# Optimization experiments

Hardware: AMD Instinct MI355X
Metric: run time of the kernel (lower is better)

The kernel has to match this reference:

```python
import jax, jax.numpy as jnp
import numpy as np

B, C, S = 32768, 30, 7
COORD, NOOBJ = 5.0, 0.5


def setup_inputs() -> dict:
    key = jax.random.key(0)
    k1, k2, k3 = jax.random.split(key, 3)
    # uniform in [0.05, 1): size loss takes sqrt of raw channels, so keep them positive
    pre = jax.random.uniform(k1, (B, C, S, S), jnp.float32, 0.05, 1.0)
    lab = jax.random.uniform(k2, (B, C, S, S), jnp.float32, 0.05, 1.0)
    # channel 4 of the label is a binary objectness indicator (code tests == 1)
    objm = (jax.random.uniform(k3, (B, S, S)) < 0.3).astype(jnp.float32)
    lab = lab.at[:, 4].set(objm)
    return {"pre": pre, "lab": lab}


def _iou(b1, b2):
    # b1, b2: [B, 4, S, S] with channels (x1, y1, x2, y2); original '+1' pixel convention
    ix1 = jnp.maximum(b1[:, 0], b2[:, 0])
    iy1 = jnp.maximum(b1[:, 1], b2[:, 1])
    ix2 = jnp.minimum(b1[:, 2], b2[:, 2])
    iy2 = jnp.minimum(b1[:, 3], b2[:, 3])
    inter = jnp.maximum(ix2 - ix1 + 1.0, 0.0) * jnp.maximum(iy2 - iy1 + 1.0, 0.0)
    a1 = (b1[:, 2] - b1[:, 0] + 1.0) * (b1[:, 3] - b1[:, 1] + 1.0)
    a2 = (b2[:, 2] - b2[:, 0] + 1.0) * (b2[:, 3] - b2[:, 1] + 1.0)
    return inter / (a1 + a2 - inter)


def reference(pre, lab):
    obj = lab[:, 4] == 1.0                      # [B,S,S] objectness mask
    iou1 = _iou(pre[:, 0:4], lab[:, 0:4])       # box 1 IoU
    iou2 = _iou(pre[:, 5:9], lab[:, 5:9])       # box 2 IoU
    resp1 = iou1 >= iou2                        # box 1 responsible

    # coordinate loss: the px*64 / py*64 grid offsets cancel in (cxl - cxp)
    addr1 = COORD * ((lab[:, 0] - pre[:, 0]) ** 2 + (lab[:, 1] - pre[:, 1]) ** 2)
    addr2 = COORD * ((lab[:, 5] - pre[:, 5]) ** 2 + (lab[:, 6] - pre[:, 6]) ** 2)

    size1 = COORD * ((jnp.sqrt(pre[:, 2]) - jnp.sqrt(lab[:, 2])) ** 2
                     + (jnp.sqrt(pre[:, 3]) - jnp.sqrt(lab[:, 3])) ** 2)
    size2 = COORD * ((jnp.sqrt(pre[:, 7]) - jnp.sqrt(lab[:, 7])) ** 2
                     + (jnp.sqrt(pre[:, 8]) - jnp.sqrt(lab[:, 8])) ** 2)

    # original always uses pre[9] as the responsible confidence (faithful to source)
    conf = NOOBJ * (pre[:, 9] - jnp.where(resp1, iou1, iou2)) ** 2

    obj_terms = jnp.where(resp1, addr1 + size1, addr2 + size2) + conf
    noobj_terms = NOOBJ * (pre[:, 4] + pre[:, 9]) ** 2

    # class loss is accumulated for every cell regardless of objectness
    cls = jnp.sum((pre[:, 10:] - lab[:, 10:]) ** 2)

    total = jnp.sum(jnp.where(obj, obj_terms, noobj_terms)) + cls
    return total / B
```

## Files before the change

### kernel.cpp

```cpp
#include <hip/hip_runtime.h>


#define BATCH   32768
#define S2      49
#define CPB     1470
#define NB      2
#define GFLOATS (NB * CPB)
#define GVEC    (GFLOATS / 4)
#define NGROUPS (BATCH / NB)
#define CELLS   (NB * S2)
#define NBLK    1536

__device__ __forceinline__ float iou4(float px1, float py1, float px2, float py2,
                                      float lx1, float ly1, float lx2, float ly2) {
    float ix1 = fmaxf(px1, lx1), iy1 = fmaxf(py1, ly1);
    float ix2 = fminf(px2, lx2), iy2 = fminf(py2, ly2);
    float iw = fmaxf(ix2 - ix1 + 1.0f, 0.0f);
    float ih = fmaxf(iy2 - iy1 + 1.0f, 0.0f);
    float inter = iw * ih;
    float a1 = (px2 - px1 + 1.0f) * (py2 - py1 + 1.0f);
    float a2 = (lx2 - lx1 + 1.0f) * (ly2 - ly1 + 1.0f);
    return inter / (a1 + a2 - inter);
}

__global__ __launch_bounds__(256) void yolo_loss_main(const float4* __restrict__ pre4,
                                                      const float4* __restrict__ lab4,
                                                      float* __restrict__ partials) {
    __shared__ float4 smem[2 * GVEC];
    __shared__ float red[4];
    float* preS = (float*)smem;
    float* labS = (float*)(smem + GVEC);
    const int tid = threadIdx.x;

    float acc = 0.0f;
    for (int g = blockIdx.x; g < NGROUPS; g += gridDim.x) {
        const float4* __restrict__ ps = pre4 + (size_t)g * GVEC;
        const float4* __restrict__ ls = lab4 + (size_t)g * GVEC;
        #pragma unroll
        for (int k = 0; k < 3; ++k) {
            int i = tid + k * 256;
            if (i < GVEC) {
                smem[i]        = ps[i];
                smem[GVEC + i] = ls[i];
            }
        }
        __syncthreads();

        if (tid < CELLS) {
            int bl = tid / S2;
            int s  = tid - bl * S2;
            const float* __restrict__ P = preS + bl * CPB + s;
            const float* __restrict__ L = labS + bl * CPB + s;

            float p0 = P[0],      p1 = P[S2],     p2 = P[2 * S2], p3 = P[3 * S2], p4 = P[4 * S2];
            float p5 = P[5 * S2], p6 = P[6 * S2], p7 = P[7 * S2], p8 = P[8 * S2], p9 = P[9 * S2];
            float l0 = L[0],      l1 = L[S2],     l2 = L[2 * S2], l3 = L[3 * S2], l4 = L[4 * S2];
            float l5 = L[5 * S2], l6 = L[6 * S2], l7 = L[7 * S2], l8 = L[8 * S2];

            float iou1 = iou4(p0, p1, p2, p3, l0, l1, l2, l3);
            float iou2 = iou4(p5, p6, p7, p8, l5, l6, l7, l8);
            bool resp1 = iou1 >= iou2;

            float d0 = l0 - p0, d1 = l1 - p1, d5 = l5 - p5, d6 = l6 - p6;
            float addr1 = 5.0f * (d0 * d0 + d1 * d1);
            float addr2 = 5.0f * (d5 * d5 + d6 * d6);

            float e2 = sqrtf(p2) - sqrtf(l2), e3 = sqrtf(p3) - sqrtf(l3);
            float e7 = sqrtf(p7) - sqrtf(l7), e8 = sqrtf(p8) - sqrtf(l8);
            float size1 = 5.0f * (e2 * e2 + e3 * e3);
            float size2 = 5.0f * (e7 * e7 + e8 * e8);

            float du = p9 - (resp1 ? iou1 : iou2);
            float conf = 0.5f * du * du;

            float obj_terms = (resp1 ? (addr1 + size1) : (addr2 + size2)) + conf;
            float pn = p4 + p9;
            float noobj = 0.5f * pn * pn;
            float cellv = (l4 == 1.0f) ? obj_terms : noobj;

            float cls = 0.0f;
            #pragma unroll
            for (int c = 10; c < 30; ++c) {
                float d = P[c * S2] - L[c * S2];
                cls += d * d;
            }
            acc += cellv + cls;
        }
        __syncthreads();
    }

    #pragma unroll
    for (int off = 32; off > 0; off >>= 1) acc += __shfl_down(acc, off);
    int lane = tid & 63, wid = tid >> 6;
    if (lane == 0) red[wid] = acc;
    __syncthreads();
    if (tid == 0) partials[blockIdx.x] = red[0] + red[1] + red[2] + red[3];
}

__global__ __launch_bounds__(256) void yolo_loss_final(const float* __restrict__ partials,
                                                       int n, float* __restrict__ out) {
    double v = 0.0;
    for (int i = (int)threadIdx.x; i < n; i += 256) v += (double)partials[i];
    __shared__ double sm[256];
    sm[threadIdx.x] = v;
    __syncthreads();
    for (int s = 128; s > 0; s >>= 1) {
        if ((int)threadIdx.x < s) sm[threadIdx.x] += sm[threadIdx.x + s];
        __syncthreads();
    }
    if (threadIdx.x == 0) out[0] = (float)(sm[0] * (1.0 / (double)BATCH));
}

extern "C" void kernel_launch(void* const* d_in, const int* in_sizes, int n_in,
                              void* d_out, int out_size, void* d_ws, size_t ws_size,
                              hipStream_t stream) {
    const float4* pre4 = (const float4*)d_in[0];
    const float4* lab4 = (const float4*)d_in[1];
    float* out = (float*)d_out;
    float* partials = (float*)d_ws;

    int nblk = NBLK;
    if (ws_size < (size_t)nblk * sizeof(float)) {
        nblk = (int)(ws_size / sizeof(float));
        if (nblk < 1) nblk = 1;
    }

    yolo_loss_main<<<nblk, 256, 0, stream>>>(pre4, lab4, partials);
    yolo_loss_final<<<1, 256, 0, stream>>>(partials, nblk, out);
}
```

Baseline: 73.01 us.

## Double-buffer LDS, stage only box channels, reduce class terms in registers

```diff
diff --git a/kernel.cpp b/kernel.cpp
--- a/kernel.cpp
+++ b/kernel.cpp
@@ -5,11 +5,13 @@
 #define S2      49
 #define CPB     1470
 #define NB      2
-#define GFLOATS (NB * CPB)
-#define GVEC    (GFLOATS / 4)
+#define GF      (NB * CPB)
+#define GV      (GF / 4)
 #define NGROUPS (BATCH / NB)
-#define CELLS   (NB * S2)
-#define NBLK    1536
+#define LDSB    492
+#define HALF    (NB * LDSB)
+#define BUFSZ   (2 * HALF)
+#define NBLK    2048
 
 __device__ __forceinline__ float iou4(float px1, float py1, float px2, float py2,
                                       float lx1, float ly1, float lx2, float ly2) {
@@ -23,70 +25,122 @@
     return inter / (a1 + a2 - inter);
 }
 
+__device__ __forceinline__ float cell_loss(const float* P, const float* L) {
+    float p0 = P[0],   p1 = P[49],  p2 = P[98],  p3 = P[147], p4 = P[196];
+    float p5 = P[245], p6 = P[294], p7 = P[343], p8 = P[392], p9 = P[441];
+    float l0 = L[0],   l1 = L[49],  l2 = L[98],  l3 = L[147], l4 = L[196];
+    float l5 = L[245], l6 = L[294], l7 = L[343], l8 = L[392];
+
+    float iou1 = iou4(p0, p1, p2, p3, l0, l1, l2, l3);
+    float iou2 = iou4(p5, p6, p7, p8, l5, l6, l7, l8);
+    bool resp1 = iou1 >= iou2;
+
+    float d0 = l0 - p0, d1 = l1 - p1, d5 = l5 - p5, d6 = l6 - p6;
+    float addr1 = 5.0f * (d0 * d0 + d1 * d1);
+    float addr2 = 5.0f * (d5 * d5 + d6 * d6);
+
+    float e2 = sqrtf(p2) - sqrtf(l2), e3 = sqrtf(p3) - sqrtf(l3);
+    float e7 = sqrtf(p7) - sqrtf(l7), e8 = sqrtf(p8) - sqrtf(l8);
+    float size1 = 5.0f * (e2 * e2 + e3 * e3);
+    float size2 = 5.0f * (e7 * e7 + e8 * e8);
+
+    float du = p9 - (resp1 ? iou1 : iou2);
+    float conf = 0.5f * du * du;
+
+    float obj_terms = (resp1 ? (addr1 + size1) : (addr2 + size2)) + conf;
+    float pn = p4 + p9;
+    float noobj = 0.5f * pn * pn;
+    return (l4 == 1.0f) ? obj_terms : noobj;
+}
+
+__device__ __forceinline__ void consume_one(float4 pv, float4 lv, int i,
+                                            float* buf, float& acc) {
+    int base = 4 * i;
+    int bl = base >= CPB;
+    int lo = base - bl * CPB;
+    if (lo <= 486) {
+        *(float4*)(buf + bl * LDSB + lo) = pv;
+        *(float4*)(buf + HALF + bl * LDSB + lo) = lv;
+    } else if (lo >= 490 && lo <= 1466) {
+        float d0 = pv.x - lv.x, d1 = pv.y - lv.y;
+        float d2 = pv.z - lv.z, d3 = pv.w - lv.w;
+        acc += d0 * d0 + d1 * d1 + d2 * d2 + d3 * d3;
+    } else {
+        float pe[4] = {pv.x, pv.y, pv.z, pv.w};
+        float le[4] = {lv.x, lv.y, lv.z, lv.w};
+        #pragma unroll
+        for (int e = 0; e < 4; ++e) {
+            int f = base + e;
+            int b2 = f >= CPB;
+            int l2 = f - b2 * CPB;
+            if (l2 < 490) {
+                buf[b2 * LDSB + l2] = pe[e];
+                buf[HALF + b2 * LDSB + l2] = le[e];
+            } else {
+                float d = pe[e] - le[e];
+                acc += d * d;
+            }
+        }
+    }
+}
+
 __global__ __launch_bounds__(256) void yolo_loss_main(const float4* __restrict__ pre4,
                                                       const float4* __restrict__ lab4,
                                                       float* __restrict__ partials) {
-    __shared__ float4 smem[2 * GVEC];
+    __shared__ __align__(16) float sbuf[2 * BUFSZ];
     __shared__ float red[4];
-    float* preS = (float*)smem;
-    float* labS = (float*)(smem + GVEC);
     const int tid = threadIdx.x;
+    float acc = 0.0f;
 
-    float acc = 0.0f;
-    for (int g = blockIdx.x; g < NGROUPS; g += gridDim.x) {
-        const float4* __restrict__ ps = pre4 + (size_t)g * GVEC;
-        const float4* __restrict__ ls = lab4 + (size_t)g * GVEC;
+    float* cb   = sbuf;
+    float* nbuf = sbuf + BUFSZ;
+
+    int g = blockIdx.x;
+    {
+        const float4* __restrict__ ps = pre4 + (size_t)g * GV;
+        const float4* __restrict__ ls = lab4 + (size_t)g * GV;
+        float4 pv[3], lv[3];
         #pragma unroll
         for (int k = 0; k < 3; ++k) {
-            int i = tid + k * 256;
-            if (i < GVEC) {
-                smem[i]        = ps[i];
-                smem[GVEC + i] = ls[i];
+            int i = tid + 256 * k;
+            if (i < GV) { pv[k] = ps[i]; lv[k] = ls[i]; }
+        }
+        #pragma unroll
+        for (int k = 0; k < 3; ++k) {
+            int i = tid + 256 * k;
+            if (i < GV) consume_one(pv[k], lv[k], i, cb, acc);
+        }
+    }
+    __syncthreads();
+
+    for (;;) {
+        int gn = g + gridDim.x;
+        bool hn = gn < NGROUPS;
+        float4 pv[3], lv[3];
+        if (hn) {
+            const float4* __restrict__ ps = pre4 + (size_t)gn * GV;
+            const float4* __restrict__ ls = lab4 + (size_t)gn * GV;
+            #pragma unroll
+            for (int k = 0; k < 3; ++k) {
+                int i = tid + 256 * k;
+                if (i < GV) { pv[k] = ps[i]; lv[k] = ls[i]; }
+            }
+        }
+        if (tid < NB * S2) {
+            int bl = tid / S2, s = tid - bl * S2;
+            acc += cell_loss(cb + bl * LDSB + s, cb + HALF + bl * LDSB + s);
+        }
+        if (hn) {
+            #pragma unroll
+            for (int k = 0; k < 3; ++k) {
+                int i = tid + 256 * k;
+                if (i < GV) consume_one(pv[k], lv[k], i, nbuf, acc);
             }
         }
         __syncthreads();
-
-        if (tid < CELLS) {
-            int bl = tid / S2;
-            int s  = tid - bl * S2;
-            const float* __restrict__ P = preS + bl * CPB + s;
-            const float* __restrict__ L = labS + bl * CPB + s;
-
-            float p0 = P[0],      p1 = P[S2],     p2 = P[2 * S2], p3 = P[3 * S2], p4 = P[4 * S2];
-            float p5 = P[5 * S2], p6 = P[6 * S2], p7 = P[7 * S2], p8 = P[8 * S2], p9 = P[9 * S2];
-            float l0 = L[0],      l1 = L[S2],     l2 = L[2 * S2], l3 = L[3 * S2], l4 = L[4 * S2];
-            float l5 = L[5 * S2], l6 = L[6 * S2], l7 = L[7 * S2], l8 = L[8 * S2];
-
-            float iou1 = iou4(p0, p1, p2, p3, l0, l1, l2, l3);
-            float iou2 = iou4(p5, p6, p7, p8, l5, l6, l7, l8);
-            bool resp1 = iou1 >= iou2;
-
-            float d0 = l0 - p0, d1 = l1 - p1, d5 = l5 - p5, d6 = l6 - p6;
-            float addr1 = 5.0f * (d0 * d0 + d1 * d1);
-            float addr2 = 5.0f * (d5 * d5 + d6 * d6);
-
-            float e2 = sqrtf(p2) - sqrtf(l2), e3 = sqrtf(p3) - sqrtf(l3);
-            float e7 = sqrtf(p7) - sqrtf(l7), e8 = sqrtf(p8) - sqrtf(l8);
-            float size1 = 5.0f * (e2 * e2 + e3 * e3);
-            float size2 = 5.0f * (e7 * e7 + e8 * e8);
-
-            float du = p9 - (resp1 ? iou1 : iou2);
-            float conf = 0.5f * du * du;
-
-            float obj_terms = (resp1 ? (addr1 + size1) : (addr2 + size2)) + conf;
-            float pn = p4 + p9;
-            float noobj = 0.5f * pn * pn;
-            float cellv = (l4 == 1.0f) ? obj_terms : noobj;
-
-            float cls = 0.0f;
-            #pragma unroll
-            for (int c = 10; c < 30; ++c) {
-                float d = P[c * S2] - L[c * S2];
-                cls += d * d;
-            }
-            acc += cellv + cls;
-        }
-        __syncthreads();
+        if (!hn) break;
+        g = gn;
+        float* t = cb; cb = nbuf; nbuf = t;
     }
 
     #pragma unroll
```

New measurement: 75.14 us. 2.9% more time.
